# Optimization experiments

Hardware: AMD Instinct MI355X
Metric: run time of the kernel (lower is better)

The kernel has to match this reference:

```python
import jax, jax.numpy as jnp
import numpy as np

FUZZY_FACTOR = 2
REG_WT = 0.0008


def setup_inputs() -> dict:
    key = jax.random.key(0)
    k1, k2 = jax.random.split(key)
    logits = jax.random.normal(k1, (2, 4, 128, 128, 128), dtype=jnp.float32)
    y_pred = jax.nn.softmax(logits, axis=1)  # module assumes softmax already applied
    image = jax.random.normal(k2, (2, 1, 128, 128, 128), dtype=jnp.float32)
    return {"y_pred": y_pred, "image": image}


def _neighbor_sum(x):
    # x: [B, K, D, H, W]; 3x3x3 ones kernel with zero center, SAME padding,
    # applied independently per (batch, cluster) channel.
    B, K, D, H, W = x.shape
    kernel = jnp.ones((1, 1, 3, 3, 3), x.dtype).at[0, 0, 1, 1, 1].set(0.0)
    y = jax.lax.conv_general_dilated(
        x.reshape(B * K, 1, D, H, W), kernel,
        window_strides=(1, 1, 1), padding="SAME",
        dimension_numbers=("NCDHW", "OIDHW", "NCDHW"))
    return y.reshape(B, K, D, H, W)


def reference(y_pred, image):
    B, K = y_pred.shape[0], y_pred.shape[1]
    N = int(np.prod(y_pred.shape[2:]))
    pred = y_pred.reshape(B, K, N)          # [B, K, N]
    img = image.reshape(B, N)               # [B, N]

    mem = pred ** FUZZY_FACTOR              # fuzzy memberships [B, K, N]

    # cluster centroids v_k = sum(img*mem)/sum(mem)  -> [B, K]
    v = jnp.sum(img[:, None, :] * mem, axis=2) / jnp.sum(mem, axis=2)

    # J_1 = sum_i mem_i * (img - v_i)^2   -> [B, N]
    J1 = jnp.sum(mem * (img[:, None, :] - v[:, :, None]) ** 2, axis=1)

    # neighbor sum of each cluster's membership map (box filter minus center)
    nb = _neighbor_sum(mem.reshape(y_pred.shape)).reshape(B, K, N)
    # sum over j != i, computed once as total - self (identical algebra)
    J_in = jnp.sum(nb, axis=1, keepdims=True) - nb  # [B, K, N]
    J2 = jnp.sum(mem * J_in, axis=1)                # [B, N]

    return jnp.mean(J1) + REG_WT * jnp.mean(J2)
```

## Files before the change

### kernel.cpp

```cpp
#include <hip/hip_runtime.h>


#define BB 2
#define KK 4
#define DD 128
#define HH 128
#define WW 128
#define PLANE (HH * WW)
#define SD 8
#define NBD (DD / SD)
#define HRB 4
#define NBH (HH / HRB)
#define NT 256

__global__ __launch_bounds__(NT) void rfcm_main(
    const float* __restrict__ yp, const float* __restrict__ img,
    double* __restrict__ ws)
{
    __shared__ double red[4 * 13];

    const int tid = threadIdx.x;
    const int wv  = tid >> 6;
    const int L   = tid & 63;
    const int c0  = L << 1;

    const int bid  = blockIdx.x;
    const int xcd  = bid & 7;
    const int idx  = bid >> 3;
    const int sl   = idx >> 5;
    const int ht   = idx & 31;
    const int slab = sl * 8 + xcd;
    const int b    = slab >> 4;
    const int dsb  = slab & 15;

    const int h  = ht * HRB + wv;
    const int d0 = dsb * SD;

    const float su = (h > 0)      ? 1.f : 0.f;
    const float sd = (h < HH - 1) ? 1.f : 0.f;
    const int   oU = (h > 0)      ? -WW : 0;
    const int   oD = (h < HH - 1) ?  WW : 0;

    const bool okL = (L > 0), okR = (L < 63);

    const float* pk[KK];
    #pragma unroll
    for (int k = 0; k < KK; k++)
        pk[k] = yp + (size_t)((b * KK + k) * DD) * PLANE + (size_t)h * WW + c0;
    const float* imgb = img + (size_t)b * DD * PLANE + (size_t)h * WW + c0;

    float2 uA[KK], oA[KK], dA[KK], uB[KK], oB[KK], dB[KK];

    auto lplane = [&](int t, float2* u, float2* o, float2* d) {
        const size_t off = (size_t)t * PLANE;
        #pragma unroll
        for (int k = 0; k < KK; k++) {
            const float* p = pk[k] + off;
            u[k] = *(const float2*)(p + oU);
            o[k] = *(const float2*)(p);
            d[k] = *(const float2*)(p + oD);
        }
    };

    auto extract = [&](const float2 u, const float2 o, const float2 dn,
                       float2& m, float2& s9) {
        m.x = o.x * o.x; m.y = o.y * o.y;
        float2 v;
        v.x = fmaf(u.x * u.x, su, fmaf(dn.x * dn.x, sd, m.x));
        v.y = fmaf(u.y * u.y, su, fmaf(dn.y * dn.y, sd, m.y));
        const float vl = okL ? __shfl_up(v.y, 1)   : 0.f;
        const float vr = okR ? __shfl_down(v.x, 1) : 0.f;
        s9.x = vl + v.x + v.y;
        s9.y = v.x + v.y + vr;
    };

    const int tp = (d0 > 0) ? d0 - 1 : d0;
    lplane(tp, uA, oA, dA);
    lplane(d0, uB, oB, dB);
    float2 iv = *(const float2*)(imgb + (size_t)d0 * PLANE);

    float2 mp[KK], sp[KK];
    float2 Mp, Sp; Mp.x = Mp.y = Sp.x = Sp.y = 0.f;
    #pragma unroll
    for (int k = 0; k < KK; k++) {
        float2 m, s9;
        extract(uA[k], oA[k], dA[k], m, s9);
        mp[k] = m; sp[k] = s9;
        Mp.x += m.x; Mp.y += m.y; Sp.x += s9.x; Sp.y += s9.y;
    }
    if (d0 == 0) {
        #pragma unroll
        for (int k = 0; k < KK; k++) {
            mp[k].x = mp[k].y = 0.f; sp[k].x = sp[k].y = 0.f;
        }
        Mp.x = Mp.y = Sp.x = Sp.y = 0.f;
    }
    lplane(d0 + 1, uA, oA, dA);

    float smf[KK] = {0,0,0,0}, sif[KK] = {0,0,0,0}, saf[KK] = {0,0,0,0};
    float j2f = 0.f;

    auto step = [&](int i, float2* uC, float2* oC, float2* dC) {
        const int t = d0 + i;
        float2 ivn = iv;
        if (i < SD - 1) ivn = *(const float2*)(imgb + (size_t)(t + 1) * PLANE);
        const bool reload = (i < SD - 2) || (i == SD - 2 && d0 + SD < DD);
        const size_t off2 = (size_t)(t + 2) * PLANE;

        const float ivx2 = iv.x * iv.x, ivy2 = iv.y * iv.y;
        float2 M, S; M.x = M.y = S.x = S.y = 0.f;
        float q = 0.f, ctt = 0.f, ctp = 0.f, cpt = 0.f;

        #pragma unroll
        for (int k = 0; k < KK; k++) {
            float2 m, s9;
            extract(uC[k], oC[k], dC[k], m, s9);
            if (reload) {
                const float* p = pk[k] + off2;
                uC[k] = *(const float2*)(p + oU);
                oC[k] = *(const float2*)(p);
                dC[k] = *(const float2*)(p + oD);
            }
            M.x += m.x; M.y += m.y; S.x += s9.x; S.y += s9.y;
            q   = fmaf(m.x, m.x,      fmaf(m.y, m.y,      q));
            ctt = fmaf(m.x, s9.x,     fmaf(m.y, s9.y,     ctt));
            ctp = fmaf(m.x, sp[k].x,  fmaf(m.y, sp[k].y,  ctp));
            if (i > 0)
                cpt = fmaf(mp[k].x, s9.x, fmaf(mp[k].y, s9.y, cpt));
            smf[k] += m.x + m.y;
            sif[k] = fmaf(m.x, iv.x, fmaf(m.y, iv.y, sif[k]));
            saf[k] = fmaf(m.x, ivx2, fmaf(m.y, ivy2, saf[k]));
            mp[k] = m; sp[k] = s9;
        }

        j2f += (M.x * S.x + M.y * S.y) - (M.x * M.x + M.y * M.y) + q - ctt
             + (M.x * Sp.x + M.y * Sp.y) - ctp;
        if (i > 0)
            j2f += (Mp.x * S.x + Mp.y * S.y) - cpt;

        Mp = M; Sp = S;
        iv = ivn;
    };

    #pragma unroll
    for (int ii = 0; ii < SD / 2; ii++) {
        step(2 * ii,     uB, oB, dB);
        step(2 * ii + 1, uA, oA, dA);
    }

    if (d0 + SD < DD) {
        float2 S; S.x = S.y = 0.f;
        float cpt = 0.f;
        #pragma unroll
        for (int k = 0; k < KK; k++) {
            float2 m, s9;
            extract(uB[k], oB[k], dB[k], m, s9);
            S.x += s9.x; S.y += s9.y;
            cpt = fmaf(mp[k].x, s9.x, fmaf(mp[k].y, s9.y, cpt));
        }
        j2f += (Mp.x * S.x + Mp.y * S.y) - cpt;
    }

    double qd[13];
    #pragma unroll
    for (int k = 0; k < KK; k++) {
        qd[k] = (double)smf[k]; qd[4 + k] = (double)sif[k]; qd[8 + k] = (double)saf[k];
    }
    qd[12] = (double)j2f;

    #pragma unroll
    for (int qq = 0; qq < 13; qq++) {
        double v = qd[qq];
        #pragma unroll
        for (int off = 32; off > 0; off >>= 1) v += __shfl_down(v, off, 64);
        qd[qq] = v;
    }

    const int lane = tid & 63, wid = tid >> 6;
    if (lane == 0) {
        #pragma unroll
        for (int qq = 0; qq < 13; qq++) red[wid * 13 + qq] = qd[qq];
    }
    __syncthreads();
    if (tid < 13) {
        const double sfin = red[tid] + red[13 + tid] + red[26 + tid] + red[39 + tid];
        int idxo;
        if      (tid < 4)  idxo = b * KK + tid;
        else if (tid < 8)  idxo = 8  + b * KK + (tid - 4);
        else if (tid < 12) idxo = 16 + b * KK + (tid - 8);
        else               idxo = 24;
        unsafeAtomicAdd(&ws[idxo], sfin);
    }
}

__global__ void rfcm_fin(const double* __restrict__ ws, float* __restrict__ out)
{
    if (threadIdx.x == 0 && blockIdx.x == 0) {
        double j1 = 0;
        #pragma unroll
        for (int i = 0; i < BB * KK; i++)
            j1 += ws[16 + i] - ws[8 + i] * ws[8 + i] / ws[i];
        const double invBN = 1.0 / ((double)BB * (double)DD * (double)HH * (double)WW);
        out[0] = (float)(j1 * invBN + 0.0008 * ws[24] * invBN);
    }
}

extern "C" void kernel_launch(void* const* d_in, const int* in_sizes, int n_in,
                              void* d_out, int out_size, void* d_ws, size_t ws_size,
                              hipStream_t stream) {
    const float* yp  = (const float*)d_in[0];
    const float* img = (const float*)d_in[1];
    float* out = (float*)d_out;
    double* ws = (double*)d_ws;

    hipMemsetAsync(d_ws, 0, 25 * sizeof(double), stream);

    dim3 grid(BB * NBD * NBH);
    rfcm_main<<<grid, NT, 0, stream>>>(yp, img, ws);
    rfcm_fin<<<1, 64, 0, stream>>>(ws, out);
}
```

Before: 132.5 us.

## Pair H rows per wave half with float4 loads and cross-half shuffles

Each wave now covers two adjacent H rows, 32 lanes per row, with each lane loading float4 (4 columns). The vertical neighbour sum shares the other row's squared membership through a xor-32 shuffle and loads only one halo row per lane, instead of loading up, own and down rows. This cuts redundant H-halo global traffic from 3x to 2x per element and widens the loads. A three-deep plane buffer replaces the two-deep one, which raises register use.

```diff
diff --git a/kernel.cpp b/kernel.cpp
--- a/kernel.cpp
+++ b/kernel.cpp
@@ -7,10 +7,11 @@
 #define HH 128
 #define WW 128
 #define PLANE (HH * WW)
+#define CL (DD * PLANE)
 #define SD 8
 #define NBD (DD / SD)
-#define HRB 4
-#define NBH (HH / HRB)
+#define HR 8
+#define NBH (HH / HR)
 #define NT 256
 
 __global__ __launch_bounds__(NT) void rfcm_main(
@@ -19,146 +20,149 @@
 {
     __shared__ double red[4 * 13];
 
-    const int tid = threadIdx.x;
-    const int wv  = tid >> 6;
-    const int L   = tid & 63;
-    const int c0  = L << 1;
+    const int tid  = threadIdx.x;
+    const int wv   = tid >> 6;
+    const int L    = tid & 63;
+    const int half = L >> 5;
+    const int wl   = L & 31;
+    const int c0   = wl << 2;
 
     const int bid  = blockIdx.x;
     const int xcd  = bid & 7;
     const int idx  = bid >> 3;
-    const int sl   = idx >> 5;
-    const int ht   = idx & 31;
+    const int sl   = idx >> 4;
+    const int ht   = idx & 15;
     const int slab = sl * 8 + xcd;
     const int b    = slab >> 4;
     const int dsb  = slab & 15;
 
-    const int h  = ht * HRB + wv;
-    const int d0 = dsb * SD;
-
-    const float su = (h > 0)      ? 1.f : 0.f;
-    const float sd = (h < HH - 1) ? 1.f : 0.f;
-    const int   oU = (h > 0)      ? -WW : 0;
-    const int   oD = (h < HH - 1) ?  WW : 0;
-
-    const bool okL = (L > 0), okR = (L < 63);
-
-    const float* pk[KK];
-    #pragma unroll
-    for (int k = 0; k < KK; k++)
-        pk[k] = yp + (size_t)((b * KK + k) * DD) * PLANE + (size_t)h * WW + c0;
-    const float* imgb = img + (size_t)b * DD * PLANE + (size_t)h * WW + c0;
-
-    float2 uA[KK], oA[KK], dA[KK], uB[KK], oB[KK], dB[KK];
-
-    auto lplane = [&](int t, float2* u, float2* o, float2* d) {
-        const size_t off = (size_t)t * PLANE;
-        #pragma unroll
-        for (int k = 0; k < KK; k++) {
-            const float* p = pk[k] + off;
-            u[k] = *(const float2*)(p + oU);
-            o[k] = *(const float2*)(p);
-            d[k] = *(const float2*)(p + oD);
+    const int rbase = ht * HR + (wv << 1);
+    const int r     = rbase + half;
+    const int d0    = dsb * SD;
+
+    const int   gr  = half ? rbase + 2 : rbase - 1;
+    const int   gH  = gr < 0 ? 0 : (gr > HH - 1 ? HH - 1 : gr);
+    const float hsc = (gr >= 0 && gr <= HH - 1) ? 1.f : 0.f;
+
+    const bool okL = (wl > 0), okR = (wl < 31);
+
+    const float* pO = yp  + (size_t)(b * KK) * CL + (size_t)r  * WW + c0;
+    const float* pH = yp  + (size_t)(b * KK) * CL + (size_t)gH * WW + c0;
+    const float* pI = img + (size_t)b * CL        + (size_t)r  * WW + c0;
+
+    float4 o0[KK], a0[KK], o1[KK], a1[KK], o2[KK], a2[KK];
+
+    auto lplane = [&](int t, float4* o, float4* a) {
+        const size_t tp = (size_t)t * PLANE;
+        #pragma unroll
+        for (int k = 0; k < KK; k++) {
+            o[k] = *(const float4*)(pO + (size_t)k * CL + tp);
+            a[k] = *(const float4*)(pH + (size_t)k * CL + tp);
         }
     };
 
-    auto extract = [&](const float2 u, const float2 o, const float2 dn,
-                       float2& m, float2& s9) {
-        m.x = o.x * o.x; m.y = o.y * o.y;
-        float2 v;
-        v.x = fmaf(u.x * u.x, su, fmaf(dn.x * dn.x, sd, m.x));
-        v.y = fmaf(u.y * u.y, su, fmaf(dn.y * dn.y, sd, m.y));
-        const float vl = okL ? __shfl_up(v.y, 1)   : 0.f;
-        const float vr = okR ? __shfl_down(v.x, 1) : 0.f;
-        s9.x = vl + v.x + v.y;
-        s9.y = v.x + v.y + vr;
+    auto extract = [&](const float4 o4, const float4 a4, float4& m, float4& s9) {
+        m.x = o4.x * o4.x; m.y = o4.y * o4.y;
+        m.z = o4.z * o4.z; m.w = o4.w * o4.w;
+        float4 v;
+        v.x = m.x + __shfl_xor(m.x, 32, 64);
+        v.y = m.y + __shfl_xor(m.y, 32, 64);
+        v.z = m.z + __shfl_xor(m.z, 32, 64);
+        v.w = m.w + __shfl_xor(m.w, 32, 64);
+        v.x = fmaf(a4.x * a4.x, hsc, v.x);
+        v.y = fmaf(a4.y * a4.y, hsc, v.y);
+        v.z = fmaf(a4.z * a4.z, hsc, v.z);
+        v.w = fmaf(a4.w * a4.w, hsc, v.w);
+        const float vl = okL ? __shfl_up(v.w, 1, 64)   : 0.f;
+        const float vr = okR ? __shfl_down(v.x, 1, 64) : 0.f;
+        const float t1 = v.x + v.y, t2 = v.z + v.w;
+        s9.x = vl + t1; s9.y = t1 + v.z; s9.z = v.y + t2; s9.w = t2 + vr;
     };
 
-    const int tp = (d0 > 0) ? d0 - 1 : d0;
-    lplane(tp, uA, oA, dA);
-    lplane(d0, uB, oB, dB);
-    float2 iv = *(const float2*)(imgb + (size_t)d0 * PLANE);
-
-    float2 mp[KK], sp[KK];
-    float2 Mp, Sp; Mp.x = Mp.y = Sp.x = Sp.y = 0.f;
+    lplane((d0 > 0) ? d0 - 1 : 0, o0, a0);
+    lplane(d0,     o1, a1);
+    lplane(d0 + 1, o2, a2);
+    float4 iv = *(const float4*)(pI + (size_t)d0 * PLANE);
+
+    float4 mp[KK], sp[KK];
+    float4 Mp = make_float4(0.f,0.f,0.f,0.f), Sp = make_float4(0.f,0.f,0.f,0.f);
     #pragma unroll
     for (int k = 0; k < KK; k++) {
-        float2 m, s9;
-        extract(uA[k], oA[k], dA[k], m, s9);
-        mp[k] = m; sp[k] = s9;
-        Mp.x += m.x; Mp.y += m.y; Sp.x += s9.x; Sp.y += s9.y;
+        extract(o0[k], a0[k], mp[k], sp[k]);
+        Mp.x += mp[k].x; Mp.y += mp[k].y; Mp.z += mp[k].z; Mp.w += mp[k].w;
+        Sp.x += sp[k].x; Sp.y += sp[k].y; Sp.z += sp[k].z; Sp.w += sp[k].w;
     }
     if (d0 == 0) {
         #pragma unroll
         for (int k = 0; k < KK; k++) {
-            mp[k].x = mp[k].y = 0.f; sp[k].x = sp[k].y = 0.f;
-        }
-        Mp.x = Mp.y = Sp.x = Sp.y = 0.f;
-    }
-    lplane(d0 + 1, uA, oA, dA);
+            mp[k] = make_float4(0.f,0.f,0.f,0.f);
+            sp[k] = make_float4(0.f,0.f,0.f,0.f);
+        }
+        Mp = make_float4(0.f,0.f,0.f,0.f); Sp = make_float4(0.f,0.f,0.f,0.f);
+    }
+    lplane(d0 + 2, o0, a0);
 
     float smf[KK] = {0,0,0,0}, sif[KK] = {0,0,0,0}, saf[KK] = {0,0,0,0};
     float j2f = 0.f;
 
-    auto step = [&](int i, float2* uC, float2* oC, float2* dC) {
+    auto step = [&](int i, float4* oS, float4* aS) {
         const int t = d0 + i;
-        float2 ivn = iv;
-        if (i < SD - 1) ivn = *(const float2*)(imgb + (size_t)(t + 1) * PLANE);
-        const bool reload = (i < SD - 2) || (i == SD - 2 && d0 + SD < DD);
-        const size_t off2 = (size_t)(t + 2) * PLANE;
-
-        const float ivx2 = iv.x * iv.x, ivy2 = iv.y * iv.y;
-        float2 M, S; M.x = M.y = S.x = S.y = 0.f;
+        float4 ivn = iv;
+        if (i < SD - 1) ivn = *(const float4*)(pI + (size_t)(t + 1) * PLANE);
+        const bool rel = (i <= SD - 3) && (t + 3 < DD);
+        const size_t tp3 = (size_t)(t + 3) * PLANE;
+
+        const float4 iv2 = make_float4(iv.x*iv.x, iv.y*iv.y, iv.z*iv.z, iv.w*iv.w);
+        float4 M = make_float4(0.f,0.f,0.f,0.f), S = make_float4(0.f,0.f,0.f,0.f);
         float q = 0.f, ctt = 0.f, ctp = 0.f, cpt = 0.f;
 
         #pragma unroll
         for (int k = 0; k < KK; k++) {
-            float2 m, s9;
-            extract(uC[k], oC[k], dC[k], m, s9);
-            if (reload) {
-                const float* p = pk[k] + off2;
-                uC[k] = *(const float2*)(p + oU);
-                oC[k] = *(const float2*)(p);
-                dC[k] = *(const float2*)(p + oD);
+            float4 m, s9;
+            extract(oS[k], aS[k], m, s9);
+            if (rel) {
+                oS[k] = *(const float4*)(pO + (size_t)k * CL + tp3);
+                aS[k] = *(const float4*)(pH + (size_t)k * CL + tp3);
             }
-            M.x += m.x; M.y += m.y; S.x += s9.x; S.y += s9.y;
-            q   = fmaf(m.x, m.x,      fmaf(m.y, m.y,      q));
-            ctt = fmaf(m.x, s9.x,     fmaf(m.y, s9.y,     ctt));
-            ctp = fmaf(m.x, sp[k].x,  fmaf(m.y, sp[k].y,  ctp));
+            M.x += m.x;  M.y += m.y;  M.z += m.z;  M.w += m.w;
+            S.x += s9.x; S.y += s9.y; S.z += s9.z; S.w += s9.w;
+            q   = fmaf(m.x,m.x,     fmaf(m.y,m.y,     fmaf(m.z,m.z,     fmaf(m.w,m.w,     q))));
+            ctt = fmaf(m.x,s9.x,    fmaf(m.y,s9.y,    fmaf(m.z,s9.z,    fmaf(m.w,s9.w,    ctt))));
+            ctp = fmaf(m.x,sp[k].x, fmaf(m.y,sp[k].y, fmaf(m.z,sp[k].z, fmaf(m.w,sp[k].w, ctp))));
             if (i > 0)
-                cpt = fmaf(mp[k].x, s9.x, fmaf(mp[k].y, s9.y, cpt));
-            smf[k] += m.x + m.y;
-            sif[k] = fmaf(m.x, iv.x, fmaf(m.y, iv.y, sif[k]));
-            saf[k] = fmaf(m.x, ivx2, fmaf(m.y, ivy2, saf[k]));
+                cpt = fmaf(mp[k].x,s9.x, fmaf(mp[k].y,s9.y, fmaf(mp[k].z,s9.z, fmaf(mp[k].w,s9.w, cpt))));
+            smf[k] += (m.x + m.y) + (m.z + m.w);
+            sif[k] = fmaf(m.x,iv.x,  fmaf(m.y,iv.y,  fmaf(m.z,iv.z,  fmaf(m.w,iv.w,  sif[k]))));
+            saf[k] = fmaf(m.x,iv2.x, fmaf(m.y,iv2.y, fmaf(m.z,iv2.z, fmaf(m.w,iv2.w, saf[k]))));
             mp[k] = m; sp[k] = s9;
         }
 
-        j2f += (M.x * S.x + M.y * S.y) - (M.x * M.x + M.y * M.y) + q - ctt
-             + (M.x * Sp.x + M.y * Sp.y) - ctp;
+        j2f += (M.x*S.x + M.y*S.y + M.z*S.z + M.w*S.w)
+             - (M.x*M.x + M.y*M.y + M.z*M.z + M.w*M.w)
+             + q - ctt
+             + (M.x*Sp.x + M.y*Sp.y + M.z*Sp.z + M.w*Sp.w) - ctp;
         if (i > 0)
-            j2f += (Mp.x * S.x + Mp.y * S.y) - cpt;
+            j2f += (Mp.x*S.x + Mp.y*S.y + Mp.z*S.z + Mp.w*S.w) - cpt;
 
         Mp = M; Sp = S;
         iv = ivn;
     };
 
-    #pragma unroll
-    for (int ii = 0; ii < SD / 2; ii++) {
-        step(2 * ii,     uB, oB, dB);
-        step(2 * ii + 1, uA, oA, dA);
-    }
+    step(0, o1, a1); step(1, o2, a2); step(2, o0, a0);
+    step(3, o1, a1); step(4, o2, a2); step(5, o0, a0);
+    step(6, o1, a1); step(7, o2, a2);
 
     if (d0 + SD < DD) {
-        float2 S; S.x = S.y = 0.f;
+        float4 S = make_float4(0.f,0.f,0.f,0.f);
         float cpt = 0.f;
         #pragma unroll
         for (int k = 0; k < KK; k++) {
-            float2 m, s9;
-            extract(uB[k], oB[k], dB[k], m, s9);
-            S.x += s9.x; S.y += s9.y;
-            cpt = fmaf(mp[k].x, s9.x, fmaf(mp[k].y, s9.y, cpt));
-        }
-        j2f += (Mp.x * S.x + Mp.y * S.y) - cpt;
+            float4 m, s9;
+            extract(o0[k], a0[k], m, s9);
+            S.x += s9.x; S.y += s9.y; S.z += s9.z; S.w += s9.w;
+            cpt = fmaf(mp[k].x,s9.x, fmaf(mp[k].y,s9.y, fmaf(mp[k].z,s9.z, fmaf(mp[k].w,s9.w, cpt))));
+        }
+        j2f += (Mp.x*S.x + Mp.y*S.y + Mp.z*S.z + Mp.w*S.w) - cpt;
     }
 
     double qd[13];
```

Result: faster. 126.8 us (median of 2 runs) (-4.3%).
